# Performance work log

Measured on AMD Instinct MI355X. Metric: run time of the kernel, lower is better.

## Reference

```python
import jax, jax.numpy as jnp
import numpy as np

N = 30000      # nodes
E = 480000     # edges per etype (avg degree 16)
IN = 256       # in_feats
OUT = 256      # out_feats
H = 4          # num_heads
DH = OUT // H  # per-head dim
K = 16         # fixed neighbor-table degree for top-5 / bottom-2 selection
ETYPES = ("rur", "rsr", "rtr")
NEG_SLOPE = 0.2


def setup_inputs() -> dict:
    key = jax.random.key(0)
    ks = iter(jax.random.split(key, 64))
    d = {"h": jax.random.normal(next(ks), (N, IN), jnp.float32)}
    for et in ETYPES:
        d[f"src_{et}"] = jax.random.randint(next(ks), (E,), 0, N)
        d[f"dst_{et}"] = jax.random.randint(next(ks), (E,), 0, N)
        d[f"ew_{et}"] = jax.random.uniform(next(ks), (E,), jnp.float32)
        d[f"nbr_idx_{et}"] = jax.random.randint(next(ks), (N, K), 0, N)
        d[f"nbr_w_{et}"] = jax.random.uniform(next(ks), (N, K), jnp.float32)
        # GATConv params: fc weight, attention vectors, bias
        d[f"W_{et}"] = jax.random.normal(next(ks), (IN, OUT), jnp.float32) / np.sqrt(IN)
        d[f"al_{et}"] = jax.random.normal(next(ks), (H, DH), jnp.float32) * 0.1
        d[f"ar_{et}"] = jax.random.normal(next(ks), (H, DH), jnp.float32) * 0.1
        d[f"b_{et}"] = jnp.zeros((OUT,), jnp.float32)
    d["Wt"] = jax.random.normal(next(ks), (OUT, 8), jnp.float32) / np.sqrt(OUT)
    d["bt"] = jnp.zeros((8,), jnp.float32)
    d["Wb"] = jax.random.normal(next(ks), (OUT, 8), jnp.float32) / np.sqrt(OUT)
    d["bb"] = jnp.zeros((8,), jnp.float32)
    d["Wp"] = jax.random.normal(next(ks), (OUT + 16, OUT), jnp.float32) / np.sqrt(OUT + 16)
    d["bp"] = jnp.zeros((OUT,), jnp.float32)
    return d


def _gat(h, src, dst, ew, W, al, ar, b):
    # DGL GATConv (eval mode): feat = h@W split into heads; additive attention;
    # edge softmax over destination; post-softmax edge_weight scaling.
    feat = (h @ W).reshape(N, H, DH)                       # [N,H,DH]
    el = (feat * al).sum(-1)                               # [N,H]
    er = (feat * ar).sum(-1)                               # [N,H]
    e = jax.nn.leaky_relu(el[src] + er[dst], NEG_SLOPE)    # [E,H]
    m = jax.ops.segment_max(e, dst, num_segments=N)        # stable softmax per dst
    ex = jnp.exp(e - m[dst])
    a = ex / jax.ops.segment_sum(ex, dst, num_segments=N)[dst]
    a = a * ew[:, None]                                    # edge_weight scaling
    msg = (a[:, :, None] * feat[src]).reshape(E, OUT)      # [E,OUT]
    return jax.ops.segment_sum(msg, dst, num_segments=N) + b


def _enhance(gat_out, nbr_idx, nbr_w, Wt, bt, Wb, bb, Wp, bp):
    # top-5 / bottom-2 neighbors by weight, mean-pooled, small MLPs, projection
    nbr_emb = gat_out[nbr_idx]                                          # [N,K,OUT]
    ti = jax.lax.top_k(nbr_w, 5)[1]                                     # [N,5]
    top5 = jnp.take_along_axis(nbr_emb, ti[:, :, None], axis=1).mean(1)
    bi = jax.lax.top_k(-nbr_w, 2)[1]                                    # [N,2]
    bot2 = jnp.take_along_axis(nbr_emb, bi[:, :, None], axis=1).mean(1)
    t = top5 @ Wt + bt                                                  # [N,8]
    bo = bot2 @ Wb + bb                                                 # [N,8]
    return jnp.concatenate([gat_out, t, bo], axis=-1) @ Wp + bp         # [N,OUT]


def reference(h,
              src_rur, dst_rur, ew_rur, nbr_idx_rur, nbr_w_rur,
              W_rur, al_rur, ar_rur, b_rur,
              src_rsr, dst_rsr, ew_rsr, nbr_idx_rsr, nbr_w_rsr,
              W_rsr, al_rsr, ar_rsr, b_rsr,
              src_rtr, dst_rtr, ew_rtr, nbr_idx_rtr, nbr_w_rtr,
              W_rtr, al_rtr, ar_rtr, b_rtr,
              Wt, bt, Wb, bb, Wp, bp):
    edges = {
        "rur": (src_rur, dst_rur, ew_rur, nbr_idx_rur, nbr_w_rur, W_rur, al_rur, ar_rur, b_rur),
        "rsr": (src_rsr, dst_rsr, ew_rsr, nbr_idx_rsr, nbr_w_rsr, W_rsr, al_rsr, ar_rsr, b_rsr),
        "rtr": (src_rtr, dst_rtr, ew_rtr, nbr_idx_rtr, nbr_w_rtr, W_rtr, al_rtr, ar_rtr, b_rtr),
    }
    outs = []
    for et in ETYPES:
        src, dst, ew, nidx, nw, W, al, ar, b = edges[et]
        g = _gat(h, src, dst, ew, W, al, ar, b)
        outs.append(_enhance(g, nidx, nw, Wt, bt, Wb, bb, Wp, bp))
    return jnp.concatenate(outs, axis=1)  # [N, 3*OUT]
```

## Files before the change

### kernel.cpp

```cpp
#include <hip/hip_runtime.h>
#include <hip/hip_fp16.h>

#define N_NODES 30000
#define N_EDGES 480000
#define NB 64
#define CHUNK 7500

typedef _Float16 f16;
typedef f16 f16x8 __attribute__((ext_vector_type(8)));
typedef float f32x4 __attribute__((ext_vector_type(4)));

__global__ void convert_h_kernel(const float* __restrict__ in, f16* __restrict__ out, int n8)
{
  int i = blockIdx.x * 256 + threadIdx.x;
  if (i >= n8) return;
  float4 a = *(const float4*)(in + (size_t)i * 8);
  float4 b = *(const float4*)(in + (size_t)i * 8 + 4);
  f16x8 v;
  v[0] = (f16)a.x; v[1] = (f16)a.y; v[2] = (f16)a.z; v[3] = (f16)a.w;
  v[4] = (f16)b.x; v[5] = (f16)b.y; v[6] = (f16)b.z; v[7] = (f16)b.w;
  *(f16x8*)(out + (size_t)i * 8) = v;
}

__global__ void transpose_w_kernel(const float* __restrict__ s0, const float* __restrict__ s1,
                                   const float* __restrict__ s2, const float* __restrict__ s3,
                                   f16* __restrict__ out)
{
  int m = blockIdx.y;
  const float* in = (m == 0) ? s0 : (m == 1) ? s1 : (m == 2) ? s2 : s3;
  int t = blockIdx.x * 256 + threadIdx.x;
  int n = t >> 8, k = t & 255;
  out[(size_t)m * 65536 + t] = (f16)in[k * 256 + n];
}

__global__ void w12_kernel(const float* __restrict__ Wp, f16* __restrict__ W12T)
{
  int t = blockIdx.x * 256 + threadIdx.x;
  if (t >= 256 * 40) return;
  int col = t / 40, k = t % 40;
  f16 v = (f16)0.f;
  if (k < 8)       v = (f16)Wp[(size_t)(256 + k) * 256 + col];
  else if (k < 16) v = (f16)Wp[(size_t)(264 + (k - 8)) * 256 + col];
  W12T[t] = v;
}

__global__ void w16_kernel(const float* __restrict__ Wt, const float* __restrict__ Wb,
                           f16* __restrict__ W16T)
{
  int t = blockIdx.x * 256 + threadIdx.x;
  if (t >= 16 * 256) return;
  int j = t >> 8, k = t & 255;
  W16T[t] = (f16)((j < 8) ? Wt[(size_t)k * 8 + j] : Wb[(size_t)k * 8 + (j - 8)]);
}

__global__ void pack_params_kernel(const float* __restrict__ al0, const float* __restrict__ al1,
                                   const float* __restrict__ al2,
                                   const float* __restrict__ ar0, const float* __restrict__ ar1,
                                   const float* __restrict__ ar2,
                                   const float* __restrict__ b0, const float* __restrict__ b1,
                                   const float* __restrict__ b2,
                                   float* __restrict__ al_all, float* __restrict__ ar_all,
                                   float* __restrict__ b_all)
{
  int et = blockIdx.x, t = threadIdx.x;
  const float* al = (et == 0) ? al0 : (et == 1) ? al1 : al2;
  const float* ar = (et == 0) ? ar0 : (et == 1) ? ar1 : ar2;
  const float* b  = (et == 0) ? b0 : (et == 1) ? b1 : b2;
  al_all[et * 256 + t] = al[t];
  ar_all[et * 256 + t] = ar[t];
  b_all[et * 256 + t]  = b[t];
}

template<int MODE>
__global__ __launch_bounds__(512)
void gemm_mfma(const f16* __restrict__ Abase, const f16* __restrict__ BTbase,
               f16* __restrict__ Chbase, float* __restrict__ Cf, int M,
               const float* __restrict__ al_all, const float* __restrict__ ar_all,
               float* __restrict__ el_all, float* __restrict__ er_all,
               const float* __restrict__ tvec_all, const float* __restrict__ bvec_all,
               const f16* __restrict__ W12Tg, const float* __restrict__ bp,
               int ldc)
{
  __shared__ alignas(16) f16 Bs[256][264];
  __shared__ alignas(16) f16 W12s[MODE ? 256 : 1][MODE ? 40 : 8];

  const int tid = threadIdx.x;
  const int et = blockIdx.y;
  const int lane = tid & 63, wv = tid >> 6;
  const int l15 = lane & 15, lq = lane >> 4;
  const int wr = wv >> 1, wc = wv & 1;
  const int bm = blockIdx.x * 128;
  const int cb = wc * 128;

  const f16* A = (MODE == 0) ? Abase : (Abase + (size_t)et * M * 256);
  const f16* BT = (MODE == 0) ? (BTbase + (size_t)et * 65536) : BTbase;

#pragma unroll
  for (int i = 0; i < 16; ++i) {
    int seg = tid + i * 512;
    int row = seg >> 5;
    int cs = (seg & 31) * 8;
    *(uint4*)&Bs[row][cs] = *(const uint4*)&BT[(size_t)row * 256 + cs];
  }
  if (MODE == 1) {
    for (int i = tid; i < 2560; i += 512)
      ((uint2*)&W12s[0][0])[i] = ((const uint2*)W12Tg)[i];
  }
  __syncthreads();

  const int r0 = bm + wr * 32 + l15;
  const int r1 = r0 + 16;
  const bool ok0 = r0 < M, ok1 = r1 < M;
  const f16* Arow0 = A + (size_t)r0 * 256;
  const f16* Arow1 = A + (size_t)r1 * 256;

  f32x4 acc[2][8] = {};

#pragma unroll
  for (int k0 = 0; k0 < 256; k0 += 32) {
    int ko = k0 + lq * 8;
    f16x8 a0 = {0, 0, 0, 0, 0, 0, 0, 0};
    f16x8 a1 = {0, 0, 0, 0, 0, 0, 0, 0};
    if (ok0) a0 = *(const f16x8*)(Arow0 + ko);
    if (ok1) a1 = *(const f16x8*)(Arow1 + ko);
#pragma unroll
    for (int nf = 0; nf < 8; ++nf) {
      f16x8 bf = *(const f16x8*)&Bs[cb + nf * 16 + l15][ko];
      acc[0][nf] = __builtin_amdgcn_mfma_f32_16x16x32_f16(a0, bf, acc[0][nf], 0, 0, 0);
      acc[1][nf] = __builtin_amdgcn_mfma_f32_16x16x32_f16(a1, bf, acc[1][nf], 0, 0, 0);
    }
  }

  if (MODE == 0) {
    f16* Ch = Chbase + (size_t)et * M * 256;
    float* el = el_all + (size_t)et * M * 4;
    float* er = er_all + (size_t)et * M * 4;
    const float* al = al_all + et * 256;
    const float* ar = ar_all + et * 256;
    float alv[8], arv[8];
#pragma unroll
    for (int nf = 0; nf < 8; ++nf) {
      alv[nf] = al[cb + nf * 16 + l15];
      arv[nf] = ar[cb + nf * 16 + l15];
    }
#pragma unroll
    for (int m = 0; m < 2; ++m)
#pragma unroll
      for (int i = 0; i < 4; ++i) {
        int row = bm + wr * 32 + m * 16 + lq * 4 + i;
        float peA = 0.f, prA = 0.f, peB = 0.f, prB = 0.f;
#pragma unroll
        for (int nf = 0; nf < 4; ++nf) {
          peA = fmaf(acc[m][nf][i], alv[nf], peA);
          prA = fmaf(acc[m][nf][i], arv[nf], prA);
          peB = fmaf(acc[m][nf + 4][i], alv[nf + 4], peB);
          prB = fmaf(acc[m][nf + 4][i], arv[nf + 4], prB);
        }
#pragma unroll
        for (int o = 8; o >= 1; o >>= 1) {
          peA += __shfl_xor(peA, o, 64);
          prA += __shfl_xor(prA, o, 64);
          peB += __shfl_xor(peB, o, 64);
          prB += __shfl_xor(prB, o, 64);
        }
        if (row < M) {
          if (l15 == 0) {
            int hA = wc * 2;
            el[row * 4 + hA] = peA;     er[row * 4 + hA] = prA;
            el[row * 4 + hA + 1] = peB; er[row * 4 + hA + 1] = prB;
          }
#pragma unroll
          for (int nf = 0; nf < 8; ++nf)
            Ch[(size_t)row * 256 + cb + nf * 16 + l15] = (f16)acc[m][nf][i];
        }
      }
  } else {
    const float* tvec = tvec_all + (size_t)et * M * 8;
    const float* bvec = bvec_all + (size_t)et * M * 8;
    const int coff = et * 256;
#pragma unroll
    for (int m = 0; m < 2; ++m) {
      int arow = bm + wr * 32 + m * 16 + l15;
      f16x8 af = {0, 0, 0, 0, 0, 0, 0, 0};
      if (arow < M && lq < 2) {
        const float* srcp = (lq == 0) ? &tvec[(size_t)arow * 8] : &bvec[(size_t)arow * 8];
        float4 x0 = *(const float4*)srcp;
        float4 x1 = *(const float4*)(srcp + 4);
        af[0] = (f16)x0.x; af[1] = (f16)x0.y; af[2] = (f16)x0.z; af[3] = (f16)x0.w;
        af[4] = (f16)x1.x; af[5] = (f16)x1.y; af[6] = (f16)x1.z; af[7] = (f16)x1.w;
      }
#pragma unroll
      for (int nf = 0; nf < 8; ++nf) {
        f16x8 bf2 = *(const f16x8*)&W12s[cb + nf * 16 + l15][lq * 8];
        acc[m][nf] = __builtin_amdgcn_mfma_f32_16x16x32_f16(af, bf2, acc[m][nf], 0, 0, 0);
      }
    }
    float bpv[8];
#pragma unroll
    for (int nf = 0; nf < 8; ++nf) bpv[nf] = bp[cb + nf * 16 + l15];
#pragma unroll
    for (int m = 0; m < 2; ++m)
#pragma unroll
      for (int i = 0; i < 4; ++i) {
        int row = bm + wr * 32 + m * 16 + lq * 4 + i;
        if (row >= M) continue;
#pragma unroll
        for (int nf = 0; nf < 8; ++nf)
          Cf[(size_t)row * ldc + coff + cb + nf * 16 + l15] = acc[m][nf][i] + bpv[nf];
      }
  }
}

__global__ __launch_bounds__(512)
void hist_kernel(const int* __restrict__ d0, const int* __restrict__ d1,
                 const int* __restrict__ d2, unsigned short* __restrict__ ghist,
                 unsigned short* __restrict__ rank16)
{
  __shared__ unsigned int h32[N_NODES / 2];
  int et = blockIdx.y, b = blockIdx.x, tid = threadIdx.x;
  const int* dst = (et == 0) ? d0 : (et == 1) ? d1 : d2;
  for (int i = tid; i < N_NODES / 2; i += 512) h32[i] = 0u;
  __syncthreads();
  int e0 = b * CHUNK;
  for (int i = tid; i < CHUNK; i += 512) {
    int e = e0 + i;
    int d = dst[e];
    unsigned int sh = (d & 1) * 16;
    unsigned int old = atomicAdd(&h32[d >> 1], 1u << sh);
    rank16[(size_t)et * N_EDGES + e] = (unsigned short)((old >> sh) & 0xFFFFu);
  }
  __syncthreads();
  unsigned short* gh = ghist + ((size_t)(et * NB + b)) * N_NODES;
  for (int d = tid; d < N_NODES; d += 512)
    gh[d] = (unsigned short)((h32[d >> 1] >> ((d & 1) * 16)) & 0xFFFFu);
}

__global__ __launch_bounds__(256)
void blockpfx_kernel(unsigned short* __restrict__ ghist, int* __restrict__ counts)
{
  int d = blockIdx.x * 256 + threadIdx.x;
  int et = blockIdx.y;
  if (d >= N_NODES) return;
  int running = 0;
#pragma unroll
  for (int b = 0; b < NB; ++b) {
    size_t idx = ((size_t)(et * NB + b)) * N_NODES + d;
    int v = ghist[idx];
    ghist[idx] = (unsigned short)running;
    running += v;
  }
  counts[et * N_NODES + d] = running;
}

__global__ __launch_bounds__(1024)
void scan_kernel(int* __restrict__ cc_all, int* __restrict__ off_all, int n, int total)
{
  int et = blockIdx.x;
  int* cc = cc_all + (size_t)et * n;
  int* off = off_all + (size_t)et * (n + 1);
  __shared__ int wsum[16];
  __shared__ int woff[16];
  __shared__ int s_carry, s_chunk;
  int tid = threadIdx.x;
  int lane = tid & 63, wid = tid >> 6;
  if (tid == 0) s_carry = 0;
  __syncthreads();
  for (int base = 0; base < n; base += 1024) {
    int i = base + tid;
    int v = (i < n) ? cc[i] : 0;
    int x = v;
#pragma unroll
    for (int s = 1; s < 64; s <<= 1) {
      int y = __shfl_up(x, s, 64);
      if (lane >= s) x += y;
    }
    if (lane == 63) wsum[wid] = x;
    __syncthreads();
    if (wid == 0 && lane < 16) {
      int ws_ = wsum[lane];
      int xx = ws_;
#pragma unroll
      for (int s = 1; s < 16; s <<= 1) {
        int y = __shfl_up(xx, s, 64);
        if (lane >= s) xx += y;
      }
      woff[lane] = xx - ws_;
      if (lane == 15) s_chunk = xx;
    }
    __syncthreads();
    int excl = s_carry + woff[wid] + (x - v);
    if (i < n) { off[i] = excl; cc[i] = excl; }
    __syncthreads();
    if (tid == 0) s_carry += s_chunk;
    __syncthreads();
  }
  if (tid == 0) off[n] = total;
}

__global__ __launch_bounds__(256)
void place_kernel(const int* __restrict__ d0, const int* __restrict__ d1,
                  const int* __restrict__ d2,
                  const int* __restrict__ s0, const int* __restrict__ s1,
                  const int* __restrict__ s2,
                  const float* __restrict__ w0, const float* __restrict__ w1,
                  const float* __restrict__ w2,
                  const int* __restrict__ off, const unsigned short* __restrict__ ghist,
                  const unsigned short* __restrict__ rank16,
                  unsigned int* __restrict__ csr_pay)
{
  int e = blockIdx.x * 256 + threadIdx.x;
  if (e >= N_EDGES) return;
  int et = blockIdx.y;
  const int* dst = (et == 0) ? d0 : (et == 1) ? d1 : d2;
  const int* src = (et == 0) ? s0 : (et == 1) ? s1 : s2;
  const float* ew = (et == 0) ? w0 : (et == 1) ? w1 : w2;
  int d = dst[e];
  int b = e / CHUNK;
  int pos = off[et * (N_NODES + 1) + d]
          + (int)ghist[((size_t)(et * NB + b)) * N_NODES + d]
          + (int)rank16[(size_t)et * N_EDGES + e];
  unsigned short hw = __half_as_ushort(__float2half_rn(ew[e]));
  csr_pay[(size_t)et * N_EDGES + pos] = (unsigned int)src[e] | ((unsigned int)hw << 16);
}

__global__ __launch_bounds__(512)
void aggregate_kernel(const int* __restrict__ off_all, const unsigned int* __restrict__ pay_all,
                      const float* __restrict__ el_all, const float* __restrict__ er_all,
                      const __half* __restrict__ feat_all, const float* __restrict__ b_all,
                      __half* __restrict__ gat_all, int n_nodes)
{
  int tid = threadIdx.x;
  int lane = tid & 63, wv = tid >> 6;
  int lg = lane >> 4, lc = lane & 15;
  int cp = blockIdx.y;
  int et = blockIdx.z;
  int n = blockIdx.x * 32 + wv * 4 + lg;
  if (n >= n_nodes) return;
  int cbase = cp * 64 + lc * 4;

  const int* off = off_all + (size_t)et * (n_nodes + 1);
  const unsigned int* csr_pay = pay_all + (size_t)et * N_EDGES;
  const float* el = el_all + (size_t)et * n_nodes * 4;
  const __half* feat = feat_all + (size_t)et * n_nodes * 256;
  const float* bias = b_all + et * 256;

  int e0 = off[n], e1 = off[n + 1];
  float ern = er_all[((size_t)et * n_nodes + n) * 4 + cp];
  float ac0 = 0.f, ac1 = 0.f, ac2 = 0.f, ac3 = 0.f, dn = 0.f;

  int e = e0;
  for (; e + 3 < e1; e += 4) {
    unsigned int p0 = csr_pay[e], p1 = csr_pay[e + 1];
    unsigned int p2 = csr_pay[e + 2], p3 = csr_pay[e + 3];
    int s0 = (int)(p0 & 0xFFFFu), s1 = (int)(p1 & 0xFFFFu);
    int s2 = (int)(p2 & 0xFFFFu), s3 = (int)(p3 & 0xFFFFu);
    float v0 = el[s0 * 4 + cp] + ern; v0 = v0 > 0.f ? v0 : 0.2f * v0;
    float v1 = el[s1 * 4 + cp] + ern; v1 = v1 > 0.f ? v1 : 0.2f * v1;
    float v2 = el[s2 * 4 + cp] + ern; v2 = v2 > 0.f ? v2 : 0.2f * v2;
    float v3 = el[s3 * 4 + cp] + ern; v3 = v3 > 0.f ? v3 : 0.2f * v3;
    float x0 = __expf(v0), x1 = __expf(v1), x2 = __expf(v2), x3 = __expf(v3);
    dn += x0 + x1 + x2 + x3;
    float c0 = x0 * __half2float(__ushort_as_half((unsigned short)(p0 >> 16)));
    float c1 = x1 * __half2float(__ushort_as_half((unsigned short)(p1 >> 16)));
    float c2 = x2 * __half2float(__ushort_as_half((unsigned short)(p2 >> 16)));
    float c3 = x3 * __half2float(__ushort_as_half((unsigned short)(p3 >> 16)));
    uint2 u0 = *(const uint2*)(feat + (size_t)s0 * 256 + cbase);
    uint2 u1 = *(const uint2*)(feat + (size_t)s1 * 256 + cbase);
    uint2 u2 = *(const uint2*)(feat + (size_t)s2 * 256 + cbase);
    uint2 u3 = *(const uint2*)(feat + (size_t)s3 * 256 + cbase);
    float2 A01 = __half22float2(*(__half2*)&u0.x), A23 = __half22float2(*(__half2*)&u0.y);
    float2 B01 = __half22float2(*(__half2*)&u1.x), B23 = __half22float2(*(__half2*)&u1.y);
    float2 C01 = __half22float2(*(__half2*)&u2.x), C23 = __half22float2(*(__half2*)&u2.y);
    float2 D01 = __half22float2(*(__half2*)&u3.x), D23 = __half22float2(*(__half2*)&u3.y);
    ac0 = fmaf(c0, A01.x, ac0); ac1 = fmaf(c0, A01.y, ac1);
    ac2 = fmaf(c0, A23.x, ac2); ac3 = fmaf(c0, A23.y, ac3);
    ac0 = fmaf(c1, B01.x, ac0); ac1 = fmaf(c1, B01.y, ac1);
    ac2 = fmaf(c1, B23.x, ac2); ac3 = fmaf(c1, B23.y, ac3);
    ac0 = fmaf(c2, C01.x, ac0); ac1 = fmaf(c2, C01.y, ac1);
    ac2 = fmaf(c2, C23.x, ac2); ac3 = fmaf(c2, C23.y, ac3);
    ac0 = fmaf(c3, D01.x, ac0); ac1 = fmaf(c3, D01.y, ac1);
    ac2 = fmaf(c3, D23.x, ac2); ac3 = fmaf(c3, D23.y, ac3);
  }
  for (; e < e1; ++e) {
    unsigned int p0 = csr_pay[e];
    int s0 = (int)(p0 & 0xFFFFu);
    float v0 = el[s0 * 4 + cp] + ern; v0 = v0 > 0.f ? v0 : 0.2f * v0;
    float x0 = __expf(v0);
    dn += x0;
    float c0 = x0 * __half2float(__ushort_as_half((unsigned short)(p0 >> 16)));
    uint2 u0 = *(const uint2*)(feat + (size_t)s0 * 256 + cbase);
    float2 A01 = __half22float2(*(__half2*)&u0.x), A23 = __half22float2(*(__half2*)&u0.y);
    ac0 = fmaf(c0, A01.x, ac0); ac1 = fmaf(c0, A01.y, ac1);
    ac2 = fmaf(c0, A23.x, ac2); ac3 = fmaf(c0, A23.y, ac3);
  }

  float invd = (dn != 0.f) ? 1.f / dn : 0.f;
  float4 bv = *(const float4*)&bias[cbase];
  __half2 h01 = __floats2half2_rn(ac0 * invd + bv.x, ac1 * invd + bv.y);
  __half2 h23 = __floats2half2_rn(ac2 * invd + bv.z, ac3 * invd + bv.w);
  uint2 st;
  st.x = *(unsigned int*)&h01;
  st.y = *(unsigned int*)&h23;
  *(uint2*)&gat_all[((size_t)et * n_nodes + n) * 256 + cbase] = st;
}

__global__ __launch_bounds__(256)
void project_mfma_kernel(const f16* __restrict__ gat, const f16* __restrict__ W16T,
                         float* __restrict__ gt, float* __restrict__ gb, int M)
{
  __shared__ alignas(16) f16 Ws[16][256];
  int tid = threadIdx.x;
  for (int i = tid; i < 512; i += 256)
    ((uint4*)&Ws[0][0])[i] = ((const uint4*)W16T)[i];
  __syncthreads();

  int lane = tid & 63, wv = tid >> 6;
  int l15 = lane & 15, lq = lane >> 4;
  int bm = blockIdx.x * 128 + wv * 32;
  int r0 = bm + l15, r1 = r0 + 16;
  bool ok0 = r0 < M, ok1 = r1 < M;

  f32x4 acc[2] = {};
#pragma unroll
  for (int k0 = 0; k0 < 256; k0 += 32) {
    int ko = k0 + lq * 8;
    f16x8 a0 = {0, 0, 0, 0, 0, 0, 0, 0};
    f16x8 a1 = {0, 0, 0, 0, 0, 0, 0, 0};
    if (ok0) a0 = *(const f16x8*)(gat + (size_t)r0 * 256 + ko);
    if (ok1) a1 = *(const f16x8*)(gat + (size_t)r1 * 256 + ko);
    f16x8 bf = *(const f16x8*)&Ws[l15][ko];
    acc[0] = __builtin_amdgcn_mfma_f32_16x16x32_f16(a0, bf, acc[0], 0, 0, 0);
    acc[1] = __builtin_amdgcn_mfma_f32_16x16x32_f16(a1, bf, acc[1], 0, 0, 0);
  }
#pragma unroll
  for (int m = 0; m < 2; ++m)
#pragma unroll
    for (int i = 0; i < 4; ++i) {
      int row = bm + m * 16 + lq * 4 + i;
      if (row >= M) continue;
      float v = acc[m][i];
      if (l15 < 8) gt[(size_t)row * 8 + l15] = v;
      else         gb[(size_t)row * 8 + (l15 - 8)] = v;
    }
}

__global__ __launch_bounds__(256)
void enhance_pool_kernel(const int* __restrict__ ni0, const int* __restrict__ ni1,
                         const int* __restrict__ ni2,
                         const float* __restrict__ nw0, const float* __restrict__ nw1,
                         const float* __restrict__ nw2,
                         const float* __restrict__ gt_all, const float* __restrict__ gb_all,
                         const float* __restrict__ bt, const float* __restrict__ bb,
                         float* __restrict__ tvec_all, float* __restrict__ bvec_all, int n_nodes)
{
  int n = (blockIdx.x * 256 + threadIdx.x) >> 6;
  int lane = threadIdx.x & 63;
  if (n >= n_nodes) return;
  int et = blockIdx.y;
  const int* nbr_idx = (et == 0) ? ni0 : (et == 1) ? ni1 : ni2;
  const float* nbr_w = (et == 0) ? nw0 : (et == 1) ? nw1 : nw2;
  const float* gt = gt_all + (size_t)et * n_nodes * 8;
  const float* gb = gb_all + (size_t)et * n_nodes * 8;
  float* tvec = tvec_all + (size_t)et * n_nodes * 8;
  float* bvec = bvec_all + (size_t)et * n_nodes * 8;
  const int l16 = lane & 15;

  float w = nbr_w[(size_t)n * 16 + l16];
  int idx = nbr_idx[(size_t)n * 16 + l16];

  int rhi = 0, rlo = 0;
#pragma unroll
  for (int i = 0; i < 16; ++i) {
    float wi = __shfl(w, i, 64);
    rhi += (wi > w) || (wi == w && i < l16);
    rlo += (wi < w) || (wi == w && i < l16);
  }

  int rows[7];
#pragma unroll
  for (int q = 0; q < 5; ++q) {
    unsigned long long m = __ballot(lane < 16 && rhi == q);
    rows[q] = __shfl(idx, __ffsll(m) - 1, 64);
  }
#pragma unroll
  for (int q = 0; q < 2; ++q) {
    unsigned long long m = __ballot(lane < 16 && rlo == q);
    rows[5 + q] = __shfl(idx, __ffsll(m) - 1, 64);
  }

  int j = lane & 7;
  if (lane < 8) {
    float s = 0.f;
#pragma unroll
    for (int q = 0; q < 5; ++q) s += gt[(size_t)rows[q] * 8 + j];
    tvec[(size_t)n * 8 + j] = s * 0.2f + bt[j];
  } else if (lane < 16) {
    float s = gb[(size_t)rows[5] * 8 + j] + gb[(size_t)rows[6] * 8 + j];
    bvec[(size_t)n * 8 + j] = s * 0.5f + bb[j];
  }
}

extern "C" void kernel_launch(void* const* d_in, const int* in_sizes, int n_in,
                              void* d_out, int out_size, void* d_ws, size_t ws_size,
                              hipStream_t stream)
{
  const int N_ = N_NODES;
  const int E_ = N_EDGES;

  const float* h = (const float*)d_in[0];
  const float* Wt = (const float*)d_in[28];
  const float* bt = (const float*)d_in[29];
  const float* Wb = (const float*)d_in[30];
  const float* bb = (const float*)d_in[31];
  const float* Wp = (const float*)d_in[32];
  const float* bp = (const float*)d_in[33];
  float* out = (float*)d_out;

  char* wsb = (char*)d_ws;
  size_t o = 0;
  auto alloc = [&](size_t bytes) -> void* {
    void* p = wsb + o;
    o = (o + bytes + 255) & ~(size_t)255;
    return p;
  };
  f16*  hf    = (f16*)alloc((size_t)N_ * 256 * 2);
  f16*  feat  = (f16*)alloc((size_t)3 * N_ * 256 * 2);
  f16*  gat   = (f16*)alloc((size_t)3 * N_ * 256 * 2);
  f16*  WT    = (f16*)alloc((size_t)4 * 256 * 256 * 2);
  f16*  W12T  = (f16*)alloc((size_t)256 * 40 * 2);
  f16*  W16T  = (f16*)alloc((size_t)16 * 256 * 2);
  float* al_all = (float*)alloc((size_t)3 * 256 * 4);
  float* ar_all = (float*)alloc((size_t)3 * 256 * 4);
  float* b_all  = (float*)alloc((size_t)3 * 256 * 4);
  float* el     = (float*)alloc((size_t)3 * N_ * 4 * 4);
  float* er     = (float*)alloc((size_t)3 * N_ * 4 * 4);
  float* gt     = (float*)alloc((size_t)3 * N_ * 8 * 4);
  float* gb     = (float*)alloc((size_t)3 * N_ * 8 * 4);
  float* tvec   = (float*)alloc((size_t)3 * N_ * 8 * 4);
  float* bvec   = (float*)alloc((size_t)3 * N_ * 8 * 4);
  int*   off    = (int*)alloc((size_t)3 * (N_ + 1) * 4);
  int*   counts = (int*)alloc((size_t)3 * N_ * 4);
  unsigned short* ghist = (unsigned short*)alloc((size_t)3 * NB * N_ * 2);
  unsigned short* rank16 = (unsigned short*)alloc((size_t)3 * E_ * 2);
  unsigned int* csr_pay = (unsigned int*)alloc((size_t)3 * E_ * 4);
  (void)ws_size; (void)in_sizes; (void)n_in; (void)out_size;

  const int row_blocks = (N_ + 127) / 128;
  const int edge_blocks = (E_ + 255) / 256;
  const int wave_blocks = (N_ + 3) / 4;
  const int agg_blocks = (N_ + 31) / 32;
  const int prj_blocks = (3 * N_ + 127) / 128;

  const int* d_dst0 = (const int*)d_in[1 + 0 * 9 + 1];
  const int* d_dst1 = (const int*)d_in[1 + 1 * 9 + 1];
  const int* d_dst2 = (const int*)d_in[1 + 2 * 9 + 1];
  const int* d_src0 = (const int*)d_in[1 + 0 * 9 + 0];
  const int* d_src1 = (const int*)d_in[1 + 1 * 9 + 0];
  const int* d_src2 = (const int*)d_in[1 + 2 * 9 + 0];
  const float* d_ew0 = (const float*)d_in[1 + 0 * 9 + 2];
  const float* d_ew1 = (const float*)d_in[1 + 1 * 9 + 2];
  const float* d_ew2 = (const float*)d_in[1 + 2 * 9 + 2];

  convert_h_kernel<<<(N_ * 256 / 8 + 255) / 256, 256, 0, stream>>>(h, hf, N_ * 256 / 8);
  transpose_w_kernel<<<dim3(256, 4), 256, 0, stream>>>(
      (const float*)d_in[1 + 0 * 9 + 5], (const float*)d_in[1 + 1 * 9 + 5],
      (const float*)d_in[1 + 2 * 9 + 5], Wp, WT);
  w12_kernel<<<(256 * 40 + 255) / 256, 256, 0, stream>>>(Wp, W12T);
  w16_kernel<<<16, 256, 0, stream>>>(Wt, Wb, W16T);
  pack_params_kernel<<<3, 256, 0, stream>>>(
      (const float*)d_in[1 + 0 * 9 + 6], (const float*)d_in[1 + 1 * 9 + 6],
      (const float*)d_in[1 + 2 * 9 + 6],
      (const float*)d_in[1 + 0 * 9 + 7], (const float*)d_in[1 + 1 * 9 + 7],
      (const float*)d_in[1 + 2 * 9 + 7],
      (const float*)d_in[1 + 0 * 9 + 8], (const float*)d_in[1 + 1 * 9 + 8],
      (const float*)d_in[1 + 2 * 9 + 8],
      al_all, ar_all, b_all);
  f16* WpT = WT + (size_t)3 * 65536;

  hist_kernel<<<dim3(NB, 3), 512, 0, stream>>>(d_dst0, d_dst1, d_dst2, ghist, rank16);
  blockpfx_kernel<<<dim3((N_ + 255) / 256, 3), 256, 0, stream>>>(ghist, counts);
  scan_kernel<<<3, 1024, 0, stream>>>(counts, off, N_, E_);
  place_kernel<<<dim3(edge_blocks, 3), 256, 0, stream>>>(
      d_dst0, d_dst1, d_dst2, d_src0, d_src1, d_src2, d_ew0, d_ew1, d_ew2,
      off, ghist, rank16, csr_pay);

  gemm_mfma<0><<<dim3(row_blocks, 3), 512, 0, stream>>>(
      hf, WT, feat, nullptr, N_, al_all, ar_all, el, er,
      nullptr, nullptr, nullptr, nullptr, 256);

  aggregate_kernel<<<dim3(agg_blocks, 4, 3), 512, 0, stream>>>(
      off, csr_pay, el, er, (const __half*)feat, b_all, (__half*)gat, N_);

  project_mfma_kernel<<<prj_blocks, 256, 0, stream>>>(
      gat, W16T, gt, gb, 3 * N_);

  enhance_pool_kernel<<<dim3(wave_blocks, 3), 256, 0, stream>>>(
      (const int*)d_in[1 + 0 * 9 + 3], (const int*)d_in[1 + 1 * 9 + 3],
      (const int*)d_in[1 + 2 * 9 + 3],
      (const float*)d_in[1 + 0 * 9 + 4], (const float*)d_in[1 + 1 * 9 + 4],
      (const float*)d_in[1 + 2 * 9 + 4],
      gt, gb, bt, bb, tvec, bvec, N_);

  gemm_mfma<1><<<dim3(row_blocks, 3), 512, 0, stream>>>(
      gat, WpT, nullptr, out, N_, nullptr, nullptr, nullptr, nullptr,
      tvec, bvec, W12T, bp, 768);
}
```

Before: 338.8 us.

## Precompute normalized per-head edge attention coefficients in separate kernel before aggregation

Adds a coef_kernel that computes each edge's softmax denominator and its normalized, edge-weighted attention per head once. It writes these as fp16 coefficients packed with the source index into a per-head payload array. The aggregate kernel then only gathers features and does FMAs, with no el gathers, exp, or denominator work. This removes redundant exp/el work repeated across the 16 lanes sharing a head, but costs an extra kernel launch, two passes over the edges, and writing then reading a 4x larger payload. Storing normalized coefficients in fp16 also lowers precision.

```diff
diff --git a/kernel.cpp b/kernel.cpp
--- a/kernel.cpp
+++ b/kernel.cpp
@@ -323,9 +323,69 @@
   csr_pay[(size_t)et * N_EDGES + pos] = (unsigned int)src[e] | ((unsigned int)hw << 16);
 }
 
+__global__ __launch_bounds__(256)
+void coef_kernel(const int* __restrict__ off_all, const unsigned int* __restrict__ pay_all,
+                 const float* __restrict__ el_all, const float* __restrict__ er_all,
+                 unsigned int* __restrict__ pay2_all, int n_nodes)
+{
+  int tid = threadIdx.x;
+  int lane = tid & 63, wv = tid >> 6;
+  int et = blockIdx.y;
+  int n = blockIdx.x * 4 + wv;
+  if (n >= n_nodes) return;
+
+  const int* off = off_all + (size_t)et * (n_nodes + 1);
+  const unsigned int* pay = pay_all + (size_t)et * N_EDGES;
+  const float* el = el_all + (size_t)et * n_nodes * 4;
+  float4 er4 = *(const float4*)(er_all + ((size_t)et * n_nodes + n) * 4);
+  int e0 = off[n], e1 = off[n + 1];
+
+  float d0 = 0.f, d1 = 0.f, d2 = 0.f, d3 = 0.f;
+  for (int e = e0 + lane; e < e1; e += 64) {
+    unsigned int p = pay[e];
+    int s = (int)(p & 0xFFFFu);
+    float4 l4 = *(const float4*)&el[(size_t)s * 4];
+    float v0 = l4.x + er4.x; v0 = v0 > 0.f ? v0 : 0.2f * v0;
+    float v1 = l4.y + er4.y; v1 = v1 > 0.f ? v1 : 0.2f * v1;
+    float v2 = l4.z + er4.z; v2 = v2 > 0.f ? v2 : 0.2f * v2;
+    float v3 = l4.w + er4.w; v3 = v3 > 0.f ? v3 : 0.2f * v3;
+    d0 += __expf(v0); d1 += __expf(v1); d2 += __expf(v2); d3 += __expf(v3);
+  }
+#pragma unroll
+  for (int o = 32; o >= 1; o >>= 1) {
+    d0 += __shfl_xor(d0, o, 64);
+    d1 += __shfl_xor(d1, o, 64);
+    d2 += __shfl_xor(d2, o, 64);
+    d3 += __shfl_xor(d3, o, 64);
+  }
+  float i0 = (d0 != 0.f) ? 1.f / d0 : 0.f;
+  float i1 = (d1 != 0.f) ? 1.f / d1 : 0.f;
+  float i2 = (d2 != 0.f) ? 1.f / d2 : 0.f;
+  float i3 = (d3 != 0.f) ? 1.f / d3 : 0.f;
+
+  for (int e = e0 + lane; e < e1; e += 64) {
+    unsigned int p = pay[e];
+    int s = (int)(p & 0xFFFFu);
+    float w = __half2float(__ushort_as_half((unsigned short)(p >> 16)));
+    float4 l4 = *(const float4*)&el[(size_t)s * 4];
+    float v0 = l4.x + er4.x; v0 = v0 > 0.f ? v0 : 0.2f * v0;
+    float v1 = l4.y + er4.y; v1 = v1 > 0.f ? v1 : 0.2f * v1;
+    float v2 = l4.z + er4.z; v2 = v2 > 0.f ? v2 : 0.2f * v2;
+    float v3 = l4.w + er4.w; v3 = v3 > 0.f ? v3 : 0.2f * v3;
+    float a0 = __expf(v0) * w * i0;
+    float a1 = __expf(v1) * w * i1;
+    float a2 = __expf(v2) * w * i2;
+    float a3 = __expf(v3) * w * i3;
+    unsigned int su = (unsigned int)s;
+    pay2_all[((size_t)(et * 4 + 0)) * N_EDGES + e] = su | ((unsigned int)__half_as_ushort(__float2half_rn(a0)) << 16);
+    pay2_all[((size_t)(et * 4 + 1)) * N_EDGES + e] = su | ((unsigned int)__half_as_ushort(__float2half_rn(a1)) << 16);
+    pay2_all[((size_t)(et * 4 + 2)) * N_EDGES + e] = su | ((unsigned int)__half_as_ushort(__float2half_rn(a2)) << 16);
+    pay2_all[((size_t)(et * 4 + 3)) * N_EDGES + e] = su | ((unsigned int)__half_as_ushort(__float2half_rn(a3)) << 16);
+  }
+}
+
 __global__ __launch_bounds__(512)
-void aggregate_kernel(const int* __restrict__ off_all, const unsigned int* __restrict__ pay_all,
-                      const float* __restrict__ el_all, const float* __restrict__ er_all,
+void aggregate_kernel(const int* __restrict__ off_all, const unsigned int* __restrict__ pay2_all,
                       const __half* __restrict__ feat_all, const float* __restrict__ b_all,
                       __half* __restrict__ gat_all, int n_nodes)
 {
@@ -339,31 +399,23 @@
   int cbase = cp * 64 + lc * 4;
 
   const int* off = off_all + (size_t)et * (n_nodes + 1);
-  const unsigned int* csr_pay = pay_all + (size_t)et * N_EDGES;
-  const float* el = el_all + (size_t)et * n_nodes * 4;
+  const unsigned int* pay2 = pay2_all + ((size_t)(et * 4 + cp)) * N_EDGES;
   const __half* feat = feat_all + (size_t)et * n_nodes * 256;
   const float* bias = b_all + et * 256;
 
   int e0 = off[n], e1 = off[n + 1];
-  float ern = er_all[((size_t)et * n_nodes + n) * 4 + cp];
-  float ac0 = 0.f, ac1 = 0.f, ac2 = 0.f, ac3 = 0.f, dn = 0.f;
+  float ac0 = 0.f, ac1 = 0.f, ac2 = 0.f, ac3 = 0.f;
 
   int e = e0;
   for (; e + 3 < e1; e += 4) {
-    unsigned int p0 = csr_pay[e], p1 = csr_pay[e + 1];
-    unsigned int p2 = csr_pay[e + 2], p3 = csr_pay[e + 3];
+    unsigned int p0 = pay2[e], p1 = pay2[e + 1];
+    unsigned int p2 = pay2[e + 2], p3 = pay2[e + 3];
     int s0 = (int)(p0 & 0xFFFFu), s1 = (int)(p1 & 0xFFFFu);
     int s2 = (int)(p2 & 0xFFFFu), s3 = (int)(p3 & 0xFFFFu);
-    float v0 = el[s0 * 4 + cp] + ern; v0 = v0 > 0.f ? v0 : 0.2f * v0;
-    float v1 = el[s1 * 4 + cp] + ern; v1 = v1 > 0.f ? v1 : 0.2f * v1;
-    float v2 = el[s2 * 4 + cp] + ern; v2 = v2 > 0.f ? v2 : 0.2f * v2;
-    float v3 = el[s3 * 4 + cp] + ern; v3 = v3 > 0.f ? v3 : 0.2f * v3;
-    float x0 = __expf(v0), x1 = __expf(v1), x2 = __expf(v2), x3 = __expf(v3);
-    dn += x0 + x1 + x2 + x3;
-    float c0 = x0 * __half2float(__ushort_as_half((unsigned short)(p0 >> 16)));
-    float c1 = x1 * __half2float(__ushort_as_half((unsigned short)(p1 >> 16)));
-    float c2 = x2 * __half2float(__ushort_as_half((unsigned short)(p2 >> 16)));
-    float c3 = x3 * __half2float(__ushort_as_half((unsigned short)(p3 >> 16)));
+    float c0 = __half2float(__ushort_as_half((unsigned short)(p0 >> 16)));
+    float c1 = __half2float(__ushort_as_half((unsigned short)(p1 >> 16)));
+    float c2 = __half2float(__ushort_as_half((unsigned short)(p2 >> 16)));
+    float c3 = __half2float(__ushort_as_half((unsigned short)(p3 >> 16)));
     uint2 u0 = *(const uint2*)(feat + (size_t)s0 * 256 + cbase);
     uint2 u1 = *(const uint2*)(feat + (size_t)s1 * 256 + cbase);
     uint2 u2 = *(const uint2*)(feat + (size_t)s2 * 256 + cbase);
@@ -382,22 +434,18 @@
     ac2 = fmaf(c3, D23.x, ac2); ac3 = fmaf(c3, D23.y, ac3);
   }
   for (; e < e1; ++e) {
-    unsigned int p0 = csr_pay[e];
+    unsigned int p0 = pay2[e];
     int s0 = (int)(p0 & 0xFFFFu);
-    float v0 = el[s0 * 4 + cp] + ern; v0 = v0 > 0.f ? v0 : 0.2f * v0;
-    float x0 = __expf(v0);
-    dn += x0;
-    float c0 = x0 * __half2float(__ushort_as_half((unsigned short)(p0 >> 16)));
+    float c0 = __half2float(__ushort_as_half((unsigned short)(p0 >> 16)));
     uint2 u0 = *(const uint2*)(feat + (size_t)s0 * 256 + cbase);
     float2 A01 = __half22float2(*(__half2*)&u0.x), A23 = __half22float2(*(__half2*)&u0.y);
     ac0 = fmaf(c0, A01.x, ac0); ac1 = fmaf(c0, A01.y, ac1);
     ac2 = fmaf(c0, A23.x, ac2); ac3 = fmaf(c0, A23.y, ac3);
   }
 
-  float invd = (dn != 0.f) ? 1.f / dn : 0.f;
   float4 bv = *(const float4*)&bias[cbase];
-  __half2 h01 = __floats2half2_rn(ac0 * invd + bv.x, ac1 * invd + bv.y);
-  __half2 h23 = __floats2half2_rn(ac2 * invd + bv.z, ac3 * invd + bv.w);
+  __half2 h01 = __floats2half2_rn(ac0 + bv.x, ac1 + bv.y);
+  __half2 h23 = __floats2half2_rn(ac2 + bv.z, ac3 + bv.w);
   uint2 st;
   st.x = *(unsigned int*)&h01;
   st.y = *(unsigned int*)&h23;
@@ -543,6 +591,7 @@
   unsigned short* ghist = (unsigned short*)alloc((size_t)3 * NB * N_ * 2);
   unsigned short* rank16 = (unsigned short*)alloc((size_t)3 * E_ * 2);
   unsigned int* csr_pay = (unsigned int*)alloc((size_t)3 * E_ * 4);
+  unsigned int* pay2 = (unsigned int*)alloc((size_t)3 * 4 * E_ * 4);
   (void)ws_size; (void)in_sizes; (void)n_in; (void)out_size;
 
   const int row_blocks = (N_ + 127) / 128;
@@ -588,8 +637,11 @@
       hf, WT, feat, nullptr, N_, al_all, ar_all, el, er,
       nullptr, nullptr, nullptr, nullptr, 256);
 
+  coef_kernel<<<dim3(wave_blocks, 3), 256, 0, stream>>>(
+      off, csr_pay, el, er, pay2, N_);
+
   aggregate_kernel<<<dim3(agg_blocks, 4, 3), 512, 0, stream>>>(
-      off, csr_pay, el, er, (const __half*)feat, b_all, (__half*)gat, N_);
+      off, pay2, (const __half*)feat, b_all, (__half*)gat, N_);
 
   project_mfma_kernel<<<prj_blocks, 256, 0, stream>>>(
       gat, W16T, gt, gb, 3 * N_);
```

Result: slower. 362.2 us (+6.9%).
